# Kernel optimization log

Measured on AMD Instinct MI355X. Metric: run time of the kernel, lower is better.

Reference implementation:

```python
import jax, jax.numpy as jnp
import numpy as np

COORD_SCALE = 10.0  # spread coords so pairwise dists span the 15/30 A cutoffs


def _cdist(x):
    # pairwise Euclidean distances for x: (b, n, 3) -> (b, n, n)
    sq = jnp.sum(x * x, axis=-1)
    d2 = sq[:, :, None] + sq[:, None, :] - 2.0 * jnp.einsum('bid,bjd->bij', x, x)
    return jnp.sqrt(jnp.clip(d2, 1e-12))  # safe sqrt (diag is 0)


def setup_inputs() -> dict:
    key = jax.random.key(0)
    k1, k2, k3, k4 = jax.random.split(key, 4)
    b, n = 2, 4096
    pred_coords = jax.random.normal(k1, (b, n, 3), dtype=jnp.float32) * COORD_SCALE
    true_coords = pred_coords + jax.random.normal(k2, (b, n, 3), dtype=jnp.float32)
    is_dna = jax.random.bernoulli(k3, 0.25, (b, n))
    is_rna = jax.random.bernoulli(k4, 0.25, (b, n))
    return {"pred_coords": pred_coords, "true_coords": true_coords,
            "is_dna": is_dna, "is_rna": is_rna}


def reference(pred_coords, true_coords, is_dna, is_rna,
              nucleic_acid_cutoff=30.0, other_cutoff=15.0):
    n = pred_coords.shape[1]
    pred_dists = _cdist(pred_coords)              # (b, n, n)
    true_dists = _cdist(true_coords)              # (b, n, n)
    dist_diff = jnp.abs(true_dists - pred_dists)
    eps = (jax.nn.sigmoid(0.5 - dist_diff) + jax.nn.sigmoid(1.0 - dist_diff)
           + jax.nn.sigmoid(2.0 - dist_diff) + jax.nn.sigmoid(4.0 - dist_diff)) / 4.0
    is_nuc = is_dna | is_rna                      # (b, n)
    is_nuc_pair = is_nuc[:, :, None] & is_nuc[:, None, :]
    inclusion = jnp.where(is_nuc_pair,
                          true_dists < nucleic_acid_cutoff,
                          true_dists < other_cutoff)
    mask = inclusion & ~jnp.eye(n, dtype=bool)[None]
    lddt_sum = jnp.sum(eps * mask, axis=(-1, -2))
    lddt_count = jnp.sum(mask, axis=(-1, -2))
    lddt = lddt_sum / jnp.maximum(lddt_count, 1).astype(lddt_sum.dtype)
    return 1.0 - jnp.mean(lddt)
```

## Files before the change

kernel.cpp:

```cpp
#include <hip/hip_runtime.h>
#include <math.h>

#define BLOCK 64

__global__ __launch_bounds__(BLOCK) void lddt_pairs(
    const float* __restrict__ pred, const float* __restrict__ truec,
    const int* __restrict__ isdna, const int* __restrict__ isrna,
    float* __restrict__ ws, int N, int C, int T)
{
  const int t = blockIdx.x;
  const int b = blockIdx.y;
  const float fC = (float)C;
  int ic = (int)((2.0f*fC + 1.0f -
                  sqrtf((2.0f*fC + 1.0f)*(2.0f*fC + 1.0f) - 8.0f*(float)t)) * 0.5f);
  if (ic > C - 1) ic = C - 1;
  if (ic < 0) ic = 0;
  while (ic > 0 && t < ic*C - ((ic*(ic-1)) >> 1)) --ic;
  while (t >= (ic+1)*C - (((ic+1)*ic) >> 1)) ++ic;
  const int jc = ic + t - (ic*C - ((ic*(ic-1)) >> 1));
  const bool diag = (ic == jc);

  __shared__ float4 sp[BLOCK];
  __shared__ float4 st[BLOCK];

  const int tid = threadIdx.x;
  {
    const int j = jc * BLOCK + tid;
    const size_t base = (size_t)b * N + j;
    const float* pp = pred  + base * 3;
    const float* tt = truec + base * 3;
    const float cutj = ((isdna[base] | isrna[base]) != 0) ? 30.0f : 15.0f;
    sp[tid] = make_float4(pp[0], pp[1], pp[2], cutj);
    st[tid] = make_float4(tt[0], tt[1], tt[2], 0.0f);
  }

  const int i = ic * BLOCK + tid;
  const size_t ibase = (size_t)b * N + i;
  const float pix = pred[ibase*3+0], piy = pred[ibase*3+1], piz = pred[ibase*3+2];
  const float tix = truec[ibase*3+0], tiy = truec[ibase*3+1], tiz = truec[ibase*3+2];
  const bool nuci = ((isdna[ibase] | isrna[ibase]) != 0);

  __syncthreads();

  const float C0 = 0.606530659712633f;
  const float C1 = 0.367879441171442f;
  const float C2 = 0.135335283236613f;
  const float C3 = 0.018315638888734f;
  const float L2E = 1.44269504088896f;

  float sum = 0.0f;
  int   cnt = 0;

  if (!diag) {
#pragma unroll 4
    for (int jj = 0; jj < BLOCK; ++jj) {
      const float4 P = sp[jj];
      const float4 T4 = st[jj];
      float dx = P.x - pix, dy = P.y - piy, dz = P.z - piz;
      float dp = __builtin_amdgcn_sqrtf(fmaf(dx, dx, fmaf(dy, dy, dz * dz)));
      float ex = T4.x - tix, ey = T4.y - tiy, ez = T4.z - tiz;
      float dt = __builtin_amdgcn_sqrtf(fmaf(ex, ex, fmaf(ey, ey, ez * ez)));

      float e = __builtin_amdgcn_exp2f(fabsf(dt - dp) * L2E);
      float u0 = fmaf(e, C0, 1.0f);
      float u1 = fmaf(e, C1, 1.0f);
      float u2 = fmaf(e, C2, 1.0f);
      float u3 = fmaf(e, C3, 1.0f);
      float s01 = u0 + u1, p01 = u0 * u1;
      float s23 = u2 + u3, p23 = u2 * u3;
      float num = fmaf(s01, p23, s23 * p01);
      float eps4 = num * __builtin_amdgcn_rcpf(p01 * p23);

      float cutoff = nuci ? P.w : 15.0f;
      bool inc = (dt < cutoff);
      unsigned long long bal = __ballot(inc);
      cnt += (int)__popcll(bal);
      sum += inc ? eps4 : 0.0f;
    }
  } else {
#pragma unroll 4
    for (int jj = 0; jj < BLOCK; ++jj) {
      const float4 P = sp[jj];
      const float4 T4 = st[jj];
      float dx = P.x - pix, dy = P.y - piy, dz = P.z - piz;
      float dp = __builtin_amdgcn_sqrtf(fmaf(dx, dx, fmaf(dy, dy, dz * dz)));
      float ex = T4.x - tix, ey = T4.y - tiy, ez = T4.z - tiz;
      float dt = __builtin_amdgcn_sqrtf(fmaf(ex, ex, fmaf(ey, ey, ez * ez)));

      float e = __builtin_amdgcn_exp2f(fabsf(dt - dp) * L2E);
      float u0 = fmaf(e, C0, 1.0f);
      float u1 = fmaf(e, C1, 1.0f);
      float u2 = fmaf(e, C2, 1.0f);
      float u3 = fmaf(e, C3, 1.0f);
      float s01 = u0 + u1, p01 = u0 * u1;
      float s23 = u2 + u3, p23 = u2 * u3;
      float num = fmaf(s01, p23, s23 * p01);
      float eps4 = num * __builtin_amdgcn_rcpf(p01 * p23);

      float cutoff = nuci ? P.w : 15.0f;
      bool inc = (dt < cutoff) && (jj != tid);
      unsigned long long bal = __ballot(inc);
      cnt += (int)__popcll(bal);
      sum += inc ? eps4 : 0.0f;
    }
  }

  for (int off = 32; off > 0; off >>= 1)
    sum += __shfl_down(sum, off, 64);

  if (tid == 0) {
    const float w = diag ? 1.0f : 2.0f;
    const int p = b * T + t;
    ws[p]         = 0.25f * w * sum;
    ws[(size_t)gridDim.y * T + p] = w * (float)cnt;
  }
}

__global__ __launch_bounds__(256) void lddt_final(
    const float* __restrict__ ws, float* __restrict__ out, int B, int T)
{
  __shared__ float rs[4], rc[4];
  float acc = 0.0f;
  for (int b = 0; b < B; ++b) {
    float s = 0.0f, c = 0.0f;
    for (int k = threadIdx.x; k < T; k += 256) {
      s += ws[b * T + k];
      c += ws[(size_t)B * T + b * T + k];
    }
    for (int off = 32; off > 0; off >>= 1) {
      s += __shfl_down(s, off, 64);
      c += __shfl_down(c, off, 64);
    }
    const int wave = threadIdx.x >> 6, lane = threadIdx.x & 63;
    if (lane == 0) { rs[wave] = s; rc[wave] = c; }
    __syncthreads();
    if (threadIdx.x == 0) {
      float S  = rs[0] + rs[1] + rs[2] + rs[3];
      float Cc = rc[0] + rc[1] + rc[2] + rc[3];
      acc += S / fmaxf(Cc, 1.0f);
    }
    __syncthreads();
  }
  if (threadIdx.x == 0) out[0] = 1.0f - acc / (float)B;
}

extern "C" void kernel_launch(void* const* d_in, const int* in_sizes, int n_in,
                              void* d_out, int out_size, void* d_ws, size_t ws_size,
                              hipStream_t stream)
{
  const float* pred  = (const float*)d_in[0];
  const float* truec = (const float*)d_in[1];
  const int*   isdna = (const int*)d_in[2];
  const int*   isrna = (const int*)d_in[3];
  float* out = (float*)d_out;
  float* ws  = (float*)d_ws;

  const int B = 2;
  const int N = in_sizes[2] / B;
  const int C = N / BLOCK;
  const int T = C * (C + 1) / 2;

  dim3 grid(T, B);
  lddt_pairs<<<grid, BLOCK, 0, stream>>>(pred, truec, isdna, isrna, ws, N, C, T);
  lddt_final<<<1, 256, 0, stream>>>(ws, out, B, T);
}
```

Measured before the change: 85.31 us.

## Fold sigmoid sum into rational polynomial, compare squared cutoffs, fuse final reduction via atomics

Coordinates are prescaled by log2(e) so the exp2 argument needs no multiply. The four-sigmoid average becomes a single quartic-over-cubic rational in e, which shortens the per-pair ALU chain. The cutoff test now uses squared distance, and the loop unroll rises from 4 to 8. The separate final reduction kernel is replaced by per-block atomics plus a last-block ticket that writes the output, with a small setup kernel to zero the accumulators. This adds contention on a few global atomics and float-atomic ordering nondeterminism.

After: 228.5 us. 168% more time.

```diff
diff --git a/kernel.cpp b/kernel.cpp
--- a/kernel.cpp
+++ b/kernel.cpp
@@ -3,10 +3,20 @@
 
 #define BLOCK 64
 
+#define L2E 1.4426950408889634f
+
+#define A1 1.1280610230094226f
+#define A2 0.3753279228541867f
+#define A3 0.0366994760193147f
+#define A4 0.0005530843701478f
+#define B1 3.3841830690282678f
+#define B2 0.7506558457083734f
+#define B3 0.0366994760193147f
+
 __global__ __launch_bounds__(BLOCK) void lddt_pairs(
     const float* __restrict__ pred, const float* __restrict__ truec,
     const int* __restrict__ isdna, const int* __restrict__ isrna,
-    float* __restrict__ ws, int N, int C, int T)
+    float* __restrict__ ws, int N, int C)
 {
   const int t = blockIdx.x;
   const int b = blockIdx.y;
@@ -20,6 +30,9 @@
   const int jc = ic + t - (ic*C - ((ic*(ic-1)) >> 1));
   const bool diag = (ic == jc);
 
+  const float C30SQ = (30.0f*L2E)*(30.0f*L2E);
+  const float C15SQ = (15.0f*L2E)*(15.0f*L2E);
+
   __shared__ float4 sp[BLOCK];
   __shared__ float4 st[BLOCK];
 
@@ -29,78 +42,62 @@
     const size_t base = (size_t)b * N + j;
     const float* pp = pred  + base * 3;
     const float* tt = truec + base * 3;
-    const float cutj = ((isdna[base] | isrna[base]) != 0) ? 30.0f : 15.0f;
-    sp[tid] = make_float4(pp[0], pp[1], pp[2], cutj);
-    st[tid] = make_float4(tt[0], tt[1], tt[2], 0.0f);
+    const float cutj2 = ((isdna[base] | isrna[base]) != 0) ? C30SQ : C15SQ;
+    sp[tid] = make_float4(pp[0]*L2E, pp[1]*L2E, pp[2]*L2E, cutj2);
+    st[tid] = make_float4(tt[0]*L2E, tt[1]*L2E, tt[2]*L2E, 0.0f);
   }
 
   const int i = ic * BLOCK + tid;
   const size_t ibase = (size_t)b * N + i;
-  const float pix = pred[ibase*3+0], piy = pred[ibase*3+1], piz = pred[ibase*3+2];
-  const float tix = truec[ibase*3+0], tiy = truec[ibase*3+1], tiz = truec[ibase*3+2];
+  const float pix = pred[ibase*3+0]*L2E, piy = pred[ibase*3+1]*L2E, piz = pred[ibase*3+2]*L2E;
+  const float tix = truec[ibase*3+0]*L2E, tiy = truec[ibase*3+1]*L2E, tiz = truec[ibase*3+2]*L2E;
   const bool nuci = ((isdna[ibase] | isrna[ibase]) != 0);
 
   __syncthreads();
-
-  const float C0 = 0.606530659712633f;
-  const float C1 = 0.367879441171442f;
-  const float C2 = 0.135335283236613f;
-  const float C3 = 0.018315638888734f;
-  const float L2E = 1.44269504088896f;
 
   float sum = 0.0f;
   int   cnt = 0;
 
   if (!diag) {
-#pragma unroll 4
+#pragma unroll 8
     for (int jj = 0; jj < BLOCK; ++jj) {
-      const float4 P = sp[jj];
+      const float4 P  = sp[jj];
       const float4 T4 = st[jj];
       float dx = P.x - pix, dy = P.y - piy, dz = P.z - piz;
       float dp = __builtin_amdgcn_sqrtf(fmaf(dx, dx, fmaf(dy, dy, dz * dz)));
       float ex = T4.x - tix, ey = T4.y - tiy, ez = T4.z - tiz;
-      float dt = __builtin_amdgcn_sqrtf(fmaf(ex, ex, fmaf(ey, ey, ez * ez)));
+      float d2t = fmaf(ex, ex, fmaf(ey, ey, ez * ez));
+      float dt = __builtin_amdgcn_sqrtf(d2t);
 
-      float e = __builtin_amdgcn_exp2f(fabsf(dt - dp) * L2E);
-      float u0 = fmaf(e, C0, 1.0f);
-      float u1 = fmaf(e, C1, 1.0f);
-      float u2 = fmaf(e, C2, 1.0f);
-      float u3 = fmaf(e, C3, 1.0f);
-      float s01 = u0 + u1, p01 = u0 * u1;
-      float s23 = u2 + u3, p23 = u2 * u3;
-      float num = fmaf(s01, p23, s23 * p01);
-      float eps4 = num * __builtin_amdgcn_rcpf(p01 * p23);
+      float e = __builtin_amdgcn_exp2f(fabsf(dt - dp));
+      float den = fmaf(fmaf(fmaf(fmaf(A4, e, A3), e, A2), e, A1), e, 1.0f);
+      float num = fmaf(fmaf(fmaf(B3, e, B2), e, B1), e, 4.0f);
+      float eps4 = num * __builtin_amdgcn_rcpf(den);
 
-      float cutoff = nuci ? P.w : 15.0f;
-      bool inc = (dt < cutoff);
-      unsigned long long bal = __ballot(inc);
-      cnt += (int)__popcll(bal);
+      float cut2 = nuci ? P.w : C15SQ;
+      bool inc = (d2t < cut2);
+      cnt += (int)__popcll(__ballot(inc));
       sum += inc ? eps4 : 0.0f;
     }
   } else {
-#pragma unroll 4
+#pragma unroll 8
     for (int jj = 0; jj < BLOCK; ++jj) {
-      const float4 P = sp[jj];
+      const float4 P  = sp[jj];
       const float4 T4 = st[jj];
       float dx = P.x - pix, dy = P.y - piy, dz = P.z - piz;
       float dp = __builtin_amdgcn_sqrtf(fmaf(dx, dx, fmaf(dy, dy, dz * dz)));
       float ex = T4.x - tix, ey = T4.y - tiy, ez = T4.z - tiz;
-      float dt = __builtin_amdgcn_sqrtf(fmaf(ex, ex, fmaf(ey, ey, ez * ez)));
+      float d2t = fmaf(ex, ex, fmaf(ey, ey, ez * ez));
+      float dt = __builtin_amdgcn_sqrtf(d2t);
 
-      float e = __builtin_amdgcn_exp2f(fabsf(dt - dp) * L2E);
-      float u0 = fmaf(e, C0, 1.0f);
-      float u1 = fmaf(e, C1, 1.0f);
-      float u2 = fmaf(e, C2, 1.0f);
-      float u3 = fmaf(e, C3, 1.0f);
-      float s01 = u0 + u1, p01 = u0 * u1;
-      float s23 = u2 + u3, p23 = u2 * u3;
-      float num = fmaf(s01, p23, s23 * p01);
-      float eps4 = num * __builtin_amdgcn_rcpf(p01 * p23);
+      float e = __builtin_amdgcn_exp2f(fabsf(dt - dp));
+      float den = fmaf(fmaf(fmaf(fmaf(A4, e, A3), e, A2), e, A1), e, 1.0f);
+      float num = fmaf(fmaf(fmaf(B3, e, B2), e, B1), e, 4.0f);
+      float eps4 = num * __builtin_amdgcn_rcpf(den);
 
-      float cutoff = nuci ? P.w : 15.0f;
-      bool inc = (dt < cutoff) && (jj != tid);
-      unsigned long long bal = __ballot(inc);
-      cnt += (int)__popcll(bal);
+      float cut2 = nuci ? P.w : C15SQ;
+      bool inc = (d2t < cut2) && (jj != tid);
+      cnt += (int)__popcll(__ballot(inc));
       sum += inc ? eps4 : 0.0f;
     }
   }
@@ -110,38 +107,31 @@
 
   if (tid == 0) {
     const float w = diag ? 1.0f : 2.0f;
-    const int p = b * T + t;
-    ws[p]         = 0.25f * w * sum;
-    ws[(size_t)gridDim.y * T + p] = w * (float)cnt;
+    atomicAdd(&ws[b],     0.25f * w * sum);
+    atomicAdd(&ws[2 + b], w * (float)cnt);
+    __threadfence();
+    unsigned* ticket = (unsigned*)(ws + 4);
+    unsigned total = gridDim.x * gridDim.y;
+    unsigned old = atomicAdd(ticket, 1u);
+    if (old == total - 1u) {
+      float s0 = atomicAdd(&ws[0], 0.0f);
+      float s1 = atomicAdd(&ws[1], 0.0f);
+      float c0 = atomicAdd(&ws[2], 0.0f);
+      float c1 = atomicAdd(&ws[3], 0.0f);
+      float lddt = 0.5f * (s0 / fmaxf(c0, 1.0f) + s1 / fmaxf(c1, 1.0f));
+      float* out = (float*)(((unsigned long long*)(ws + 8))[0]);
+      out[0] = 1.0f - lddt;
+    }
   }
 }
 
-__global__ __launch_bounds__(256) void lddt_final(
-    const float* __restrict__ ws, float* __restrict__ out, int B, int T)
+__global__ void lddt_setptr(float* ws, float* out)
 {
-  __shared__ float rs[4], rc[4];
-  float acc = 0.0f;
-  for (int b = 0; b < B; ++b) {
-    float s = 0.0f, c = 0.0f;
-    for (int k = threadIdx.x; k < T; k += 256) {
-      s += ws[b * T + k];
-      c += ws[(size_t)B * T + b * T + k];
-    }
-    for (int off = 32; off > 0; off >>= 1) {
-      s += __shfl_down(s, off, 64);
-      c += __shfl_down(c, off, 64);
-    }
-    const int wave = threadIdx.x >> 6, lane = threadIdx.x & 63;
-    if (lane == 0) { rs[wave] = s; rc[wave] = c; }
-    __syncthreads();
-    if (threadIdx.x == 0) {
-      float S  = rs[0] + rs[1] + rs[2] + rs[3];
-      float Cc = rc[0] + rc[1] + rc[2] + rc[3];
-      acc += S / fmaxf(Cc, 1.0f);
-    }
-    __syncthreads();
+  if (threadIdx.x == 0) {
+    ((unsigned long long*)(ws + 8))[0] = (unsigned long long)out;
+    ws[0] = 0.0f; ws[1] = 0.0f; ws[2] = 0.0f; ws[3] = 0.0f;
+    ((unsigned*)(ws + 4))[0] = 0u;
   }
-  if (threadIdx.x == 0) out[0] = 1.0f - acc / (float)B;
 }
 
 extern "C" void kernel_launch(void* const* d_in, const int* in_sizes, int n_in,
@@ -160,7 +150,8 @@
   const int C = N / BLOCK;
   const int T = C * (C + 1) / 2;
 
+  lddt_setptr<<<1, 64, 0, stream>>>(ws, out);
+
   dim3 grid(T, B);
-  lddt_pairs<<<grid, BLOCK, 0, stream>>>(pred, truec, isdna, isrna, ws, N, C, T);
-  lddt_final<<<1, 256, 0, stream>>>(ws, out, B, T);
+  lddt_pairs<<<grid, BLOCK, 0, stream>>>(pred, truec, isdna, isrna, ws, N, C);
 }
```
